# Kernel tuning notes

Hardware: AMD Instinct MI355X
Metric: run time of the kernel (lower is better)

The kernel has to match this reference:

```python
import jax, jax.numpy as jnp
import numpy as np

B, V, C, H, W = 4, 5, 32, 256, 320
COSTNUM, GROUPS = 4, 8


def _rodrigues(w):
    theta = np.linalg.norm(w) + 1e-12
    k = w / theta
    K = np.array([[0, -k[2], k[1]], [k[2], 0, -k[0]], [-k[1], k[0], 0]], np.float64)
    return (np.eye(3) + np.sin(theta) * K + (1 - np.cos(theta)) * (K @ K)).astype(np.float32)


def setup_inputs() -> dict:
    key = jax.random.key(0)
    k1, k2, k3 = jax.random.split(key, 3)
    features = jax.random.normal(k1, (B, V, C, H, W), jnp.float32)
    # DTU-style metric depths in [425, 935]
    depth_values = 425.0 + 510.0 * jax.random.uniform(k2, (B, 1, H, W), jnp.float32)
    # per-pixel inverse-depth interval (Inverse=True path samples in 1/depth space)
    depth_interval = jnp.ones((B, 1, H, W), jnp.float32) * 2e-4
    view_weights = jax.random.uniform(k3, (B, V - 1, H, W), jnp.float32)
    rng = np.random.default_rng(0)
    f = 300.0
    K4 = np.eye(4, dtype=np.float32)
    K4[:3, :3] = np.array([[f, 0, W / 2], [0, f, H / 2], [0, 0, 1]], np.float32)
    projs = np.zeros((B, V, 2, 4, 4), np.float32)
    for b in range(B):
        for v in range(V):
            E = np.eye(4, dtype=np.float32)
            if v > 0:  # small relative pose for source views
                E[:3, :3] = _rodrigues(0.02 * rng.standard_normal(3))
                E[:3, 3] = 5.0 * rng.standard_normal(3)
            projs[b, v, 0] = E   # extrinsics 4x4
            projs[b, v, 1] = K4  # intrinsics in top-left 3x3
    return {
        "depth_values": depth_values,
        "features": features,
        "proj_matrices": jnp.asarray(projs),
        "depth_interval": depth_interval,
        "depth_max": jnp.full((1,), 935.0, jnp.float32),
        "depth_min": jnp.full((1,), 425.0, jnp.float32),
        "view_weights": view_weights,
        "CostNum": COSTNUM,
        "G": GROUPS,
    }


def _bilinear(src, gx, gy):
    # src: [C, H, W]; gx, gy: [N] pixel coords; zeros padding, align_corners=True
    Hh, Ww = src.shape[1], src.shape[2]
    x0 = jnp.floor(gx)
    y0 = jnp.floor(gy)
    wx1 = gx - x0
    wy1 = gy - y0

    def gather(xi, yi):
        valid = (xi >= 0) & (xi <= Ww - 1) & (yi >= 0) & (yi <= Hh - 1)
        xc = jnp.clip(xi, 0, Ww - 1).astype(jnp.int32)
        yc = jnp.clip(yi, 0, Hh - 1).astype(jnp.int32)
        return src[:, yc, xc] * valid.astype(src.dtype)  # [C, N]

    return (gather(x0, y0) * ((1 - wx1) * (1 - wy1))
            + gather(x0 + 1, y0) * (wx1 * (1 - wy1))
            + gather(x0, y0 + 1) * ((1 - wx1) * wy1)
            + gather(x0 + 1, y0 + 1) * (wx1 * wy1))


def _homo_warp(src_fea, src_proj, ref_proj, depth_samples):
    # src_fea [B,C,H,W]; projs [B,4,4]; depth_samples [B,D,H,W]
    Bn, Cc, Hh, Ww = src_fea.shape
    D = depth_samples.shape[1]
    dt = src_fea.dtype
    proj = jnp.einsum('bij,bjk->bik', src_proj, jnp.linalg.inv(ref_proj))
    rot, trans = proj[:, :3, :3], proj[:, :3, 3]
    y, x = jnp.meshgrid(jnp.arange(Hh, dtype=dt), jnp.arange(Ww, dtype=dt), indexing='ij')
    xyz = jnp.stack([x.ravel(), y.ravel(), jnp.ones(Hh * Ww, dt)], 0)  # [3, HW]
    rot_xyz = jnp.einsum('bij,jn->bin', rot, xyz)  # [B,3,HW]
    pts = rot_xyz[:, :, None, :] * depth_samples.reshape(Bn, 1, D, Hh * Ww) + trans[:, :, None, None]
    # grid computed under no_grad in the torch original -> stop_gradient
    gx = jax.lax.stop_gradient(pts[:, 0] / pts[:, 2]).reshape(Bn, -1)
    gy = jax.lax.stop_gradient(pts[:, 1] / pts[:, 2]).reshape(Bn, -1)
    warped = jax.vmap(_bilinear)(src_fea, gx, gy)  # [B, C, D*HW]
    return warped.reshape(Bn, Cc, D, Hh, Ww)


def _depth_range_samples(cur_depth, ndepth, interval):
    # cur_depth, interval: [B,H,W] (inverse-depth space here)
    dmin = cur_depth - ndepth / 2 * interval
    dmax = cur_depth + ndepth / 2 * interval
    step = (dmax - dmin) / (ndepth - 1)
    idx = jnp.arange(ndepth, dtype=cur_depth.dtype).reshape(1, -1, 1, 1)
    return dmin[:, None] + idx * step[:, None]  # [B, D, H, W]


def _proj_new(p):
    # p: [B,2,4,4]; fold intrinsics into extrinsics: top 3x4 = K[:3,:3] @ E[:3,:4]
    top = jnp.einsum('bij,bjk->bik', p[:, 1, :3, :3], p[:, 0, :3, :4])
    return p[:, 0].at[:, :3, :4].set(top)


def reference(depth_values, features, proj_matrices, depth_interval, depth_max, depth_min, view_weights, CostNum, G):
    Bn, Vn, Cc, Hh, Ww = features.shape
    ref_feature = features[:, 0]
    # Inverse=True: sample uniformly in inverse-depth space
    inv_depth = 1.0 / depth_values[:, 0]
    samples = _depth_range_samples(inv_depth, CostNum, depth_interval[:, 0])
    samples = 1.0 / samples  # back to metric depth, [B, D, H, W]

    ref_proj_new = _proj_new(proj_matrices[:, 0])
    ref_g = ref_feature.reshape(Bn, G, Cc // G, Hh, Ww)

    sim_sum = jnp.zeros((Bn, G, CostNum, Hh, Ww), ref_feature.dtype)
    w_sum = jnp.zeros((Bn, 1, 1, Hh, Ww), ref_feature.dtype)
    for i in range(1, Vn):
        src_proj_new = _proj_new(proj_matrices[:, i])
        warped = _homo_warp(features[:, i], src_proj_new, ref_proj_new, samples)
        warped = warped.reshape(Bn, G, Cc // G, CostNum, Hh, Ww)
        sim = (warped * ref_g[:, :, :, None]).mean(2)  # [B, G, D, H, W]
        vw = view_weights[:, i - 1][:, None, None]  # [B,1,1,H,W]
        sim_sum = sim_sum + sim * vw
        w_sum = w_sum + vw
    similarity = sim_sum / (w_sum + 1e-6)
    similarity = similarity.reshape(Bn, G * CostNum, Hh, Ww)
    return similarity, samples
```

## Files before the change

kernel.cpp:

```cpp
#include <hip/hip_runtime.h>
#include <math.h>

#define Bn 4
#define Vn 5
#define Cc 32
#define Hh 256
#define Ww 320
#define DD 4
#define GG 8
#define HW (Hh*Ww)
#define BLOCKS_PER_B (HW/256)
#define NXCD 8
#define BAND (Bn * BLOCKS_PER_B / NXCD)
#define NCHUNK 4

__global__ void proj_kernel(const float* __restrict__ proj, float* __restrict__ out12) {
    int t = blockIdx.x * blockDim.x + threadIdx.x;
    if (t >= Bn * (Vn - 1)) return;
    int b = t / (Vn - 1);
    int i = t % (Vn - 1) + 1;

    const float* pb = proj + (size_t)b * Vn * 2 * 16;

    double refm[16], srcm[16];
    {
        const float* E = pb + 0 * 32 + 0;
        const float* K = pb + 0 * 32 + 16;
        for (int r = 0; r < 3; r++)
            for (int c = 0; c < 4; c++) {
                double s = 0.0;
                for (int k = 0; k < 3; k++) s += (double)K[r*4+k] * (double)E[k*4+c];
                refm[r*4+c] = s;
            }
        for (int c = 0; c < 4; c++) refm[12+c] = (double)E[12+c];
    }
    {
        const float* E = pb + i * 32 + 0;
        const float* K = pb + i * 32 + 16;
        for (int r = 0; r < 3; r++)
            for (int c = 0; c < 4; c++) {
                double s = 0.0;
                for (int k = 0; k < 3; k++) s += (double)K[r*4+k] * (double)E[k*4+c];
                srcm[r*4+c] = s;
            }
        for (int c = 0; c < 4; c++) srcm[12+c] = (double)E[12+c];
    }

    double a[16], inv[16];
    for (int k = 0; k < 16; k++) { a[k] = refm[k]; inv[k] = 0.0; }
    inv[0] = inv[5] = inv[10] = inv[15] = 1.0;
    for (int col = 0; col < 4; col++) {
        int piv = col; double best = fabs(a[col*4+col]);
        for (int r = col + 1; r < 4; r++) {
            double v = fabs(a[r*4+col]);
            if (v > best) { best = v; piv = r; }
        }
        if (piv != col) {
            for (int c = 0; c < 4; c++) {
                double tmp = a[col*4+c]; a[col*4+c] = a[piv*4+c]; a[piv*4+c] = tmp;
                tmp = inv[col*4+c]; inv[col*4+c] = inv[piv*4+c]; inv[piv*4+c] = tmp;
            }
        }
        double rd = 1.0 / a[col*4+col];
        for (int c = 0; c < 4; c++) { a[col*4+c] *= rd; inv[col*4+c] *= rd; }
        for (int r = 0; r < 4; r++) {
            if (r == col) continue;
            double f = a[r*4+col];
            for (int c = 0; c < 4; c++) { a[r*4+c] -= f * a[col*4+c]; inv[r*4+c] -= f * inv[col*4+c]; }
        }
    }

    double P[16];
    for (int r = 0; r < 4; r++)
        for (int c = 0; c < 4; c++) {
            double s = 0.0;
            for (int k = 0; k < 4; k++) s += srcm[r*4+k] * inv[k*4+c];
            P[r*4+c] = s;
        }

    float* o = out12 + t * 12;
    o[0] = (float)P[0];  o[1] = (float)P[1];  o[2]  = (float)P[2];
    o[3] = (float)P[4];  o[4] = (float)P[5];  o[5]  = (float)P[6];
    o[6] = (float)P[8];  o[7] = (float)P[9];  o[8]  = (float)P[10];
    o[9] = (float)P[3];  o[10] = (float)P[7]; o[11] = (float)P[11];
}

__global__ __launch_bounds__(256) void cost_kernel(
    const float* __restrict__ depth_values,
    const float* __restrict__ features,
    const float* __restrict__ depth_interval,
    const float* __restrict__ view_weights,
    const float* __restrict__ P12,
    float* __restrict__ sim_out,
    float* __restrict__ samp_out)
{
    int bid   = blockIdx.x;
    int xcd   = bid & (NXCD - 1);
    int s     = bid >> 3;
    int pbb   = s >> 2;
    int chunk = s & 3;
    int unit  = xcd * BAND + pbb;
    int b     = unit / BLOCKS_PER_B;
    int pb    = unit - b * BLOCKS_PER_B;
    int c0    = chunk * 8;

    int pix = pb * 256 + threadIdx.x;
    int h   = pix / Ww;
    int w   = pix - h * Ww;

    float inv_d = 1.0f / depth_values[b * HW + pix];
    float itv   = depth_interval[b * HW + pix];
    float dmin  = inv_d - 2.0f * itv;
    float step  = (4.0f * itv) / 3.0f;

    float depth[DD];
    #pragma unroll
    for (int d = 0; d < DD; d++) {
        float sdi = dmin + (float)d * step;
        depth[d] = 1.0f / sdi;
    }
    if (chunk == 0) {
        #pragma unroll
        for (int d = 0; d < DD; d++)
            __builtin_nontemporal_store(depth[d],
                &samp_out[((size_t)b * DD + d) * HW + pix]);
    }

    float vw[Vn - 1];
    float wsum = 0.0f;
    #pragma unroll
    for (int i = 0; i < Vn - 1; i++) {
        vw[i] = view_weights[((size_t)b * (Vn - 1) + i) * HW + pix];
        wsum += vw[i];
    }
    float dn = 1.0f / (wsum + 1e-6f);

    const float xf = (float)w, yf = (float)h;
    const float* refp = features + (size_t)b * Vn * Cc * HW + pix;
    float* so_base = sim_out + (size_t)b * (GG * DD) * HW + pix;

    float ref8[8];
    #pragma unroll
    for (int j = 0; j < 8; j++) ref8[j] = refp[(size_t)(c0 + j) * HW];

    float acc[2][DD];
    #pragma unroll
    for (int g2 = 0; g2 < 2; g2++)
        #pragma unroll
        for (int d = 0; d < DD; d++) acc[g2][d] = 0.0f;

    #pragma unroll 1
    for (int i = 0; i < Vn - 1; i++) {
        const float* P = P12 + (b * (Vn - 1) + i) * 12;
        float rx = P[0] * xf + P[1] * yf + P[2];
        float ry = P[3] * xf + P[4] * yf + P[5];
        float rz = P[6] * xf + P[7] * yf + P[8];
        float tx = P[9], ty = P[10], tz = P[11];

        float scale = 0.25f * vw[i];
        const float* src = features + ((size_t)(b * Vn) + (i + 1)) * Cc * HW
                         + (size_t)c0 * HW;

        #pragma unroll
        for (int d = 0; d < DD; d++) {
            float D  = depth[d];
            float px = rx * D + tx;
            float py = ry * D + ty;
            float pz = rz * D + tz;
            float rpz = 1.0f / pz;
            float gx = px * rpz;
            float gy = py * rpz;

            float x0f = floorf(gx);
            float y0f = floorf(gy);
            float wx1 = gx - x0f;
            float wy1 = gy - y0f;
            float wx0 = 1.0f - wx1;
            float wy0 = 1.0f - wy1;

            float xbf = fminf(fmaxf(x0f, 0.0f), (float)(Ww - 2));
            float ybf = fminf(fmaxf(y0f, 0.0f), (float)(Hh - 2));
            float dxf = x0f - xbf;
            float dyf = y0f - ybf;

            float pcx0 = (dxf == 0.0f) ? wx0 : ((dxf == -1.0f) ? wx1 : 0.0f);
            float pcx1 = (dxf == 0.0f) ? wx1 : ((dxf ==  1.0f) ? wx0 : 0.0f);
            float pcy0 = (dyf == 0.0f) ? wy0 : ((dyf == -1.0f) ? wy1 : 0.0f);
            float pcy1 = (dyf == 0.0f) ? wy1 : ((dyf ==  1.0f) ? wy0 : 0.0f);

            float W00 = pcx0 * pcy0 * scale;
            float W10 = pcx1 * pcy0 * scale;
            float W01 = pcx0 * pcy1 * scale;
            float W11 = pcx1 * pcy1 * scale;

            int o00 = (int)ybf * Ww + (int)xbf;

            #pragma unroll
            for (int j = 0; j < 8; j++) {
                const float* p = src + (size_t)j * HW + o00;
                float val = W00 * p[0] + W10 * p[1] + W01 * p[Ww] + W11 * p[Ww + 1];
                acc[j >> 2][d] += val * ref8[j];
            }
        }
    }

    #pragma unroll
    for (int g2 = 0; g2 < 2; g2++)
        #pragma unroll
        for (int d = 0; d < DD; d++)
            __builtin_nontemporal_store(acc[g2][d] * dn,
                &so_base[(size_t)(((c0 >> 2) + g2) * DD + d) * HW]);
}

extern "C" void kernel_launch(void* const* d_in, const int* in_sizes, int n_in,
                              void* d_out, int out_size, void* d_ws, size_t ws_size,
                              hipStream_t stream) {
    const float* depth_values   = (const float*)d_in[0];
    const float* features       = (const float*)d_in[1];
    const float* projm          = (const float*)d_in[2];
    const float* depth_interval = (const float*)d_in[3];
    const float* view_weights   = (const float*)d_in[6];

    float* out      = (float*)d_out;
    float* sim_out  = out;
    float* samp_out = out + (size_t)Bn * GG * DD * HW;
    float* P12      = (float*)d_ws;

    proj_kernel<<<1, 64, 0, stream>>>(projm, P12);
    cost_kernel<<<Bn * NCHUNK * BLOCKS_PER_B, 256, 0, stream>>>(
        depth_values, features, depth_interval, view_weights, P12, sim_out, samp_out);
}
```

Baseline: 521.6 us.

## Transpose source features to channel-last and process all channels per thread

Adds a transpose kernel that rewrites the source-view features into a pixel-major, 32-channel-contiguous layout in workspace, so each bilinear corner becomes a few float4 loads instead of strided per-channel gathers. The cost kernel now handles all 32 channels per thread and drops the 4-way channel chunking, so projection math and weight computation are done once per pixel. In exchange it pays an extra full read and write of the source features each call, needs a large workspace, and raises register pressure. The old kernel remains as a fallback when the workspace is too small.

```diff
diff --git a/kernel.cpp b/kernel.cpp
--- a/kernel.cpp
+++ b/kernel.cpp
@@ -14,6 +14,9 @@
 #define BAND (Bn * BLOCKS_PER_B / NXCD)
 #define NCHUNK 4
 
+#define FT_OFFSET 1024
+#define FT_BYTES ((size_t)Bn * 4 * HW * 32 * 4)
+
 __global__ void proj_kernel(const float* __restrict__ proj, float* __restrict__ out12) {
     int t = blockIdx.x * blockDim.x + threadIdx.x;
     if (t >= Bn * (Vn - 1)) return;
@@ -85,7 +88,157 @@
     o[9] = (float)P[3];  o[10] = (float)P[7]; o[11] = (float)P[11];
 }
 
-__global__ __launch_bounds__(256) void cost_kernel(
+__global__ __launch_bounds__(256) void transpose_kernel(
+    const float* __restrict__ features, float* __restrict__ ft)
+{
+    int t   = blockIdx.x * 256 + threadIdx.x;
+    int b   = t / (4 * HW);
+    int r   = t - b * 4 * HW;
+    int v   = r / HW;
+    int pix = r - v * HW;
+
+    const float* src = features + ((size_t)(b * Vn + (v + 1)) * Cc) * HW + pix;
+    float* dst = ft + (size_t)t * 32;
+
+    #pragma unroll
+    for (int q = 0; q < 8; q++) {
+        float4 o;
+        o.x = src[(size_t)(q * 4 + 0) * HW];
+        o.y = src[(size_t)(q * 4 + 1) * HW];
+        o.z = src[(size_t)(q * 4 + 2) * HW];
+        o.w = src[(size_t)(q * 4 + 3) * HW];
+        *reinterpret_cast<float4*>(dst + q * 4) = o;
+    }
+}
+
+__global__ __launch_bounds__(256) void cost_kernel_t(
+    const float* __restrict__ depth_values,
+    const float* __restrict__ features,
+    const float* __restrict__ ft,
+    const float* __restrict__ depth_interval,
+    const float* __restrict__ view_weights,
+    const float* __restrict__ P12,
+    float* __restrict__ sim_out,
+    float* __restrict__ samp_out)
+{
+    int bid  = blockIdx.x;
+    int xcd  = bid & (NXCD - 1);
+    int s    = bid >> 3;
+    int unit = xcd * BAND + s;
+    int b    = unit / BLOCKS_PER_B;
+    int pb   = unit - b * BLOCKS_PER_B;
+    int pix  = pb * 256 + threadIdx.x;
+    int h    = pix / Ww;
+    int w    = pix - h * Ww;
+
+    float inv_d = 1.0f / depth_values[b * HW + pix];
+    float itv   = depth_interval[b * HW + pix];
+    float dmin  = inv_d - 2.0f * itv;
+    float step  = (4.0f * itv) / 3.0f;
+
+    float depth[DD];
+    #pragma unroll
+    for (int d = 0; d < DD; d++) {
+        float sdi = dmin + (float)d * step;
+        depth[d] = 1.0f / sdi;
+        __builtin_nontemporal_store(depth[d],
+            &samp_out[((size_t)b * DD + d) * HW + pix]);
+    }
+
+    float vw[Vn - 1];
+    float wsum = 0.0f;
+    #pragma unroll
+    for (int i = 0; i < Vn - 1; i++) {
+        vw[i] = view_weights[((size_t)b * (Vn - 1) + i) * HW + pix];
+        wsum += vw[i];
+    }
+    float dn = 1.0f / (wsum + 1e-6f);
+
+    const float xf = (float)w, yf = (float)h;
+    const float* refp = features + (size_t)b * Vn * Cc * HW + pix;
+    float* so_base = sim_out + (size_t)b * (GG * DD) * HW + pix;
+
+    float ref32[32];
+    #pragma unroll
+    for (int c = 0; c < 32; c++) ref32[c] = refp[(size_t)c * HW];
+
+    float acc[GG][DD];
+    #pragma unroll
+    for (int g = 0; g < GG; g++)
+        #pragma unroll
+        for (int d = 0; d < DD; d++) acc[g][d] = 0.0f;
+
+    #pragma unroll 1
+    for (int i = 0; i < Vn - 1; i++) {
+        const float* P = P12 + (b * (Vn - 1) + i) * 12;
+        float rx = P[0] * xf + P[1] * yf + P[2];
+        float ry = P[3] * xf + P[4] * yf + P[5];
+        float rz = P[6] * xf + P[7] * yf + P[8];
+        float tx = P[9], ty = P[10], tz = P[11];
+
+        float scale = 0.25f * vw[i];
+        const float* src = ft + ((size_t)(b * 4 + i) * HW) * 32;
+
+        #pragma unroll
+        for (int d = 0; d < DD; d++) {
+            float D  = depth[d];
+            float px = rx * D + tx;
+            float py = ry * D + ty;
+            float pz = rz * D + tz;
+            float rpz = 1.0f / pz;
+            float gx = px * rpz;
+            float gy = py * rpz;
+
+            float x0f = floorf(gx);
+            float y0f = floorf(gy);
+            float wx1 = gx - x0f;
+            float wy1 = gy - y0f;
+            float wx0 = 1.0f - wx1;
+            float wy0 = 1.0f - wy1;
+
+            float xbf = fminf(fmaxf(x0f, 0.0f), (float)(Ww - 2));
+            float ybf = fminf(fmaxf(y0f, 0.0f), (float)(Hh - 2));
+            float dxf = x0f - xbf;
+            float dyf = y0f - ybf;
+
+            float pcx0 = (dxf == 0.0f) ? wx0 : ((dxf == -1.0f) ? wx1 : 0.0f);
+            float pcx1 = (dxf == 0.0f) ? wx1 : ((dxf ==  1.0f) ? wx0 : 0.0f);
+            float pcy0 = (dyf == 0.0f) ? wy0 : ((dyf == -1.0f) ? wy1 : 0.0f);
+            float pcy1 = (dyf == 0.0f) ? wy1 : ((dyf ==  1.0f) ? wy0 : 0.0f);
+
+            float W00 = pcx0 * pcy0 * scale;
+            float W10 = pcx1 * pcy0 * scale;
+            float W01 = pcx0 * pcy1 * scale;
+            float W11 = pcx1 * pcy1 * scale;
+
+            int o00 = (int)ybf * Ww + (int)xbf;
+            const float* p00 = src + (size_t)o00 * 32;
+
+            #pragma unroll
+            for (int q = 0; q < GG; q++) {
+                float4 A = *reinterpret_cast<const float4*>(p00 + q * 4);
+                float4 Bq = *reinterpret_cast<const float4*>(p00 + 32 + q * 4);
+                float4 Cq = *reinterpret_cast<const float4*>(p00 + Ww * 32 + q * 4);
+                float4 Dq = *reinterpret_cast<const float4*>(p00 + Ww * 32 + 32 + q * 4);
+                float v0 = W00 * A.x + W10 * Bq.x + W01 * Cq.x + W11 * Dq.x;
+                float v1 = W00 * A.y + W10 * Bq.y + W01 * Cq.y + W11 * Dq.y;
+                float v2 = W00 * A.z + W10 * Bq.z + W01 * Cq.z + W11 * Dq.z;
+                float v3 = W00 * A.w + W10 * Bq.w + W01 * Cq.w + W11 * Dq.w;
+                acc[q][d] += v0 * ref32[q*4+0] + v1 * ref32[q*4+1]
+                           + v2 * ref32[q*4+2] + v3 * ref32[q*4+3];
+            }
+        }
+    }
+
+    #pragma unroll
+    for (int g = 0; g < GG; g++)
+        #pragma unroll
+        for (int d = 0; d < DD; d++)
+            __builtin_nontemporal_store(acc[g][d] * dn,
+                &so_base[(size_t)(g * DD + d) * HW]);
+}
+
+__global__ __launch_bounds__(256) void cost_kernel_fb(
     const float* __restrict__ depth_values,
     const float* __restrict__ features,
     const float* __restrict__ depth_interval,
@@ -227,6 +380,16 @@
     float* P12      = (float*)d_ws;
 
     proj_kernel<<<1, 64, 0, stream>>>(projm, P12);
-    cost_kernel<<<Bn * NCHUNK * BLOCKS_PER_B, 256, 0, stream>>>(
-        depth_values, features, depth_interval, view_weights, P12, sim_out, samp_out);
-}
+
+    if (ws_size >= (size_t)FT_OFFSET + FT_BYTES) {
+        float* ft = (float*)((char*)d_ws + FT_OFFSET);
+        transpose_kernel<<<Bn * 4 * BLOCKS_PER_B, 256, 0, stream>>>(features, ft);
+        cost_kernel_t<<<Bn * BLOCKS_PER_B, 256, 0, stream>>>(
+            depth_values, features, ft, depth_interval, view_weights,
+            P12, sim_out, samp_out);
+    } else {
+        cost_kernel_fb<<<Bn * NCHUNK * BLOCKS_PER_B, 256, 0, stream>>>(
+            depth_values, features, depth_interval, view_weights,
+            P12, sim_out, samp_out);
+    }
+}
```

New measurement: 721.2 us. 38.3% more time.
